# Performance work log

Measured on AMD Instinct MI355X. Metric: run time of the kernel, lower is better.

## Reference

```python
import jax, jax.numpy as jnp
import numpy as np

N, D = 16384, 256

def setup_inputs() -> dict:
    key = jax.random.key(0)
    k1, k2 = jax.random.split(key)
    image_emb = jax.random.normal(k1, (N, D), dtype=jnp.float32)
    text_emb = jax.random.normal(k2, (N, D), dtype=jnp.float32)
    return {"image_emb": image_emb, "text_emb": text_emb}

def reference(image_emb, text_emb):
    n = image_emb.shape[0]
    # [n, n] similarity logits
    logits = image_emb @ text_emb.T
    labels = jnp.arange(n)
    # cross-entropy with diagonal labels: -log_softmax(logits)[i, i]
    logp_t = jax.nn.log_softmax(logits, axis=-1)        # image -> text (rows)
    logp_i = jax.nn.log_softmax(logits.T, axis=-1)      # text -> image (cols)
    loss_t = -logp_t[labels, labels]
    loss_i = -logp_i[labels, labels]
    loss = ((loss_i + loss_t) * 0.5).mean()
    return loss
```

## Files before the change

### kernel.cpp

```cpp
#include <hip/hip_runtime.h>
#include <hip/hip_bf16.h>

#define NN 16384
#define DD 256

typedef unsigned short u16;
typedef unsigned int u32;
typedef unsigned char u8;
typedef long i64;
typedef __attribute__((ext_vector_type(4))) float f32x4;
typedef __attribute__((ext_vector_type(4))) int i32x4;
typedef __attribute__((ext_vector_type(8))) int i32x8;

__global__ __launch_bounds__(256) void prep_kernel(
        const float* __restrict__ img, const float* __restrict__ txt,
        u8* __restrict__ A8, u8* __restrict__ B8,
        float* __restrict__ zbuf ,
        float* __restrict__ out) {
    __shared__ u32 sA[16 * 65 + 8];
    __shared__ u32 sB[16 * 65 + 8];
    const int t = threadIdx.x, bi = blockIdx.x;
    const float4* ib = (const float4*)img + ((size_t)bi << 10);
    const float4* tb = (const float4*)txt + ((size_t)bi << 10);
    const float S = 1.44269504088896f;
    #pragma unroll
    for (int k = 0; k < 4; ++k) {
        const int idx = (k << 8) + t;
        const int row = idx >> 6, col = idx & 63;
        float4 va = ib[idx];
        int pa = __builtin_amdgcn_cvt_pk_fp8_f32(va.x * S, va.y * S, 0, false);
        pa     = __builtin_amdgcn_cvt_pk_fp8_f32(va.z * S, va.w * S, pa, true);
        sA[row * 65 + col] = (u32)pa;
        float4 vb = tb[idx];
        int pb = __builtin_amdgcn_cvt_pk_fp8_f32(vb.x, vb.y, 0, false);
        pb     = __builtin_amdgcn_cvt_pk_fp8_f32(vb.z, vb.w, pb, true);
        sB[row * 65 + col] = (u32)pb;
    }
    __syncthreads();
    const int w = t >> 6, l = t & 63;
    const int k2 = w >> 1, jj = w & 1, qq = l >> 4, mm = l & 15;
    const int wb = mm * 65 + (k2 << 5) + (qq << 3) + (jj << 2);
    i32x4 oa = { (int)sA[wb], (int)sA[wb + 1], (int)sA[wb + 2], (int)sA[wb + 3] };
    i32x4 ob = { (int)sB[wb], (int)sB[wb + 1], (int)sB[wb + 2], (int)sB[wb + 3] };
    const size_t dst = ((size_t)(bi >> 3) << 15) + (k2 << 14) + ((size_t)(bi & 7) << 11)
                     + (jj << 10) + (qq << 8) + (mm << 4);
    *(i32x4*)(A8 + dst) = oa;
    *(i32x4*)(B8 + dst) = ob;
    const int gid = (bi << 8) + t;
    if (gid < 32768) zbuf[gid] = 0.0f;
    if (gid == 0) out[0] = 0.0f;
}

__global__ __launch_bounds__(256, 2) void gemm_lse_kernel(
        const u8* __restrict__ A8, const u8* __restrict__ B8,
        float* __restrict__ s_row, float* __restrict__ s_col,
        float* __restrict__ diag) {
    const int t = threadIdx.x;
    const int lane = t & 63;
    const int w = t >> 6;
    const int wr = w >> 1, wc = w & 1;
    const int q = lane >> 4, m = lane & 15;
    const int bi = blockIdx.x & 127;
    const int jg = blockIdx.x >> 7;
    const int row0 = bi << 7;

    const u8* Aw = A8 + ((size_t)bi << 15) + ((size_t)lane << 4);
    i32x8 areg[2][4];
    #pragma unroll
    for (int k2 = 0; k2 < 2; ++k2)
        #pragma unroll
        for (int rb = 0; rb < 4; ++rb) {
            const u8* p = Aw + (k2 << 14) + (((wr << 2) + rb) << 11);
            i32x4 lo = *(const i32x4*)(p);
            i32x4 hi = *(const i32x4*)(p + 1024);
            areg[k2][rb] = __builtin_shufflevector(lo, hi, 0, 1, 2, 3, 4, 5, 6, 7);
        }

    const f32x4 fzero = {0.f, 0.f, 0.f, 0.f};
    f32x4 accA[4][2], accB[4][2];
    f32x4 rp[4] = {fzero, fzero, fzero, fzero};
    float cpartT = 0.0f;

    const u8* Bw = B8 + (wc << 13) + ((size_t)lane << 4);

    i32x8 bfX[4], bfY[4];

    auto load_half = [&](i32x8 (&bf)[4], int jt_, int h) {
        const int ct = (jg << 4) | ((jt_ + bi) & 15);
        const u8* p = Bw + ((size_t)ct << 15) + (h << 12);
        #pragma unroll
        for (int k2 = 0; k2 < 2; ++k2) {
            const u8* pp = p + (k2 << 14);
            i32x4 lo0 = *(const i32x4*)(pp);
            i32x4 hi0 = *(const i32x4*)(pp + 1024);
            bf[k2 * 2 + 0] = __builtin_shufflevector(lo0, hi0, 0, 1, 2, 3, 4, 5, 6, 7);
            i32x4 lo1 = *(const i32x4*)(pp + 2048);
            i32x4 hi1 = *(const i32x4*)(pp + 3072);
            bf[k2 * 2 + 1] = __builtin_shufflevector(lo1, hi1, 0, 1, 2, 3, 4, 5, 6, 7);
        }
    };

    auto mfma_half = [&](f32x4 (&acc)[4][2], i32x8 (&bf)[4]) {
        const f32x4 cinit = {-144.f, -144.f, -144.f, -144.f};
        #pragma unroll
        for (int rb = 0; rb < 4; ++rb) {
            acc[rb][0] = __builtin_amdgcn_mfma_scale_f32_16x16x128_f8f6f4(
                areg[0][rb], bf[0], cinit, 0, 0, 0, 127, 0, 127);
            acc[rb][1] = __builtin_amdgcn_mfma_scale_f32_16x16x128_f8f6f4(
                areg[0][rb], bf[1], cinit, 0, 0, 0, 127, 0, 127);
        }
        #pragma unroll
        for (int rb = 0; rb < 4; ++rb) {
            acc[rb][0] = __builtin_amdgcn_mfma_scale_f32_16x16x128_f8f6f4(
                areg[1][rb], bf[2], acc[rb][0], 0, 0, 0, 127, 0, 127);
            acc[rb][1] = __builtin_amdgcn_mfma_scale_f32_16x16x128_f8f6f4(
                areg[1][rb], bf[3], acc[rb][1], 0, 0, 0, 127, 0, 127);
        }
    };

    auto epilogue_half = [&](f32x4 (&acc)[4][2], int jt_, int h) {
        const int ct = (jg << 4) | ((jt_ + bi) & 15);
        if (bi == ct && wr == wc) {
            #pragma unroll
            for (int rb = 0; rb < 4; ++rb)
                if ((rb >> 1) == h) {
                    #pragma unroll
                    for (int r = 0; r < 4; ++r)
                        if (m == ((q << 2) | r))
                            diag[row0 + (wr << 6) + (rb << 4) + m] = acc[rb][rb & 1][r];
                }
        }
        #pragma unroll
        for (int rb = 0; rb < 4; ++rb)
            #pragma unroll
            for (int cb = 0; cb < 2; ++cb)
                #pragma unroll
                for (int r = 0; r < 4; ++r)
                    acc[rb][cb][r] = __builtin_amdgcn_exp2f(acc[rb][cb][r]);
        #pragma unroll
        for (int rb = 0; rb < 4; ++rb)
            rp[rb] += acc[rb][0] + acc[rb][1];
        #pragma unroll
        for (int cb = 0; cb < 2; ++cb) {
            f32x4 s = (acc[0][cb] + acc[1][cb]) + (acc[2][cb] + acc[3][cb]);
            float v = (s[0] + s[1]) + (s[2] + s[3]);
            v += __shfl_xor(v, 16, 64);
            v += __shfl_xor(v, 32, 64);
            if (q == ((h << 1) | cb)) cpartT = v;
        }
        if (h == 1) {
            const int col0 = ct << 7;
            atomicAdd(&s_col[col0 + (wc << 6) + (q << 4) + m], cpartT);
        }
    };

    load_half(bfX, 0, 0);
    load_half(bfY, 0, 1);
    mfma_half(accA, bfX);
    load_half(bfX, 1, 0);
    mfma_half(accB, bfY);
    epilogue_half(accA, 0, 0);
    #pragma unroll 1
    for (int jt = 1; jt < 16; ++jt) {
        load_half(bfY, jt, 1);
        mfma_half(accA, bfX);
        epilogue_half(accB, jt - 1, 1);
        if (jt < 15) load_half(bfX, jt + 1, 0);
        mfma_half(accB, bfY);
        epilogue_half(accA, jt, 0);
    }
    epilogue_half(accB, 15, 1);

    float rout = 0.0f;
    #pragma unroll
    for (int rb = 0; rb < 4; ++rb)
        #pragma unroll
        for (int r = 0; r < 4; ++r) {
            float v = rp[rb][r];
            v += __shfl_xor(v, 1, 16);
            v += __shfl_xor(v, 2, 16);
            v += __shfl_xor(v, 4, 16);
            v += __shfl_xor(v, 8, 16);
            if (m == ((rb << 2) | r)) rout = v;
        }
    atomicAdd(&s_row[row0 + (wr << 6) + ((m >> 2) << 4) + (q << 2) + (m & 3)], rout);
}

__global__ void final_kernel(const float* __restrict__ s_row, const float* __restrict__ s_col,
                             const float* __restrict__ diag, float* __restrict__ out) {
    __shared__ double red[256];
    int t = threadIdx.x;
    int i = blockIdx.x * 256 + t;
    double p = 0.5 * (double)(log2f(s_row[i]) + log2f(s_col[i])) - (double)diag[i];
    red[t] = p;
    __syncthreads();
    for (int s = 128; s > 0; s >>= 1) {
        if (t < s) red[t] += red[t + s];
        __syncthreads();
    }
    if (t == 0) atomicAdd(out, (float)(red[0] * 0.6931471805599453 / (double)NN));
}

extern "C" void kernel_launch(void* const* d_in, const int* in_sizes, int n_in,
                              void* d_out, int out_size, void* d_ws, size_t ws_size,
                              hipStream_t stream) {
    const float* img = (const float*)d_in[0];
    const float* txt = (const float*)d_in[1];
    char* ws = (char*)d_ws;
    u8*    A8    = (u8*)ws;
    u8*    B8    = (u8*)(ws + 4194304);
    float* s_row = (float*)(ws + 8388608);
    float* s_col = (float*)(ws + 8388608 + 65536);
    float* diag  = (float*)(ws + 8388608 + 131072);
    float* out   = (float*)d_out;

    prep_kernel<<<1024, 256, 0, stream>>>(img, txt, A8, B8, s_row, out);
    gemm_lse_kernel<<<1024, 256, 0, stream>>>(A8, B8, s_row, s_col, diag);
    final_kernel<<<64, 256, 0, stream>>>(s_row, s_col, diag, out);
}
```

Measured before the change: 155.8 us.

## Warp-specialize GEMM-LSE kernel into MFMA producer and exp consumer warps

Splits each 512-thread block into four MFMA producer waves and four epilogue consumer waves. Producers write accumulator tiles to two LDS buffers, and consumers apply exp2 and the row/column reductions, with __syncthreads handing tiles between them. The grid shrinks to 256 blocks, each walking 64 column tiles instead of 16, so column-sum atomics per block rise while grid count falls. The aim is to overlap transcendental and reduction work with matrix math. In exchange it adds two block-wide barriers per tile and 64KB of LDS per block, which may cap occupancy and serialize the two roles.

```diff
diff --git a/kernel.cpp b/kernel.cpp
--- a/kernel.cpp
+++ b/kernel.cpp
@@ -51,139 +51,167 @@
     if (gid == 0) out[0] = 0.0f;
 }
 
-__global__ __launch_bounds__(256, 2) void gemm_lse_kernel(
+__global__ __launch_bounds__(512, 2) void gemm_lse_kernel(
         const u8* __restrict__ A8, const u8* __restrict__ B8,
         float* __restrict__ s_row, float* __restrict__ s_col,
         float* __restrict__ diag) {
+    __shared__ float hbuf0[8192];
+    __shared__ float hbuf1[8192];
+
     const int t = threadIdx.x;
     const int lane = t & 63;
     const int w = t >> 6;
-    const int wr = w >> 1, wc = w & 1;
+    const int pw = w & 3;
+    const int wr = pw >> 1, wc = pw & 1;
     const int q = lane >> 4, m = lane & 15;
     const int bi = blockIdx.x & 127;
     const int jg = blockIdx.x >> 7;
     const int row0 = bi << 7;
 
-    const u8* Aw = A8 + ((size_t)bi << 15) + ((size_t)lane << 4);
-    i32x8 areg[2][4];
-    #pragma unroll
-    for (int k2 = 0; k2 < 2; ++k2)
+    if (w < 4) {
+        const u8* Aw = A8 + ((size_t)bi << 15) + ((size_t)lane << 4);
+        i32x8 areg[2][4];
         #pragma unroll
-        for (int rb = 0; rb < 4; ++rb) {
-            const u8* p = Aw + (k2 << 14) + (((wr << 2) + rb) << 11);
-            i32x4 lo = *(const i32x4*)(p);
-            i32x4 hi = *(const i32x4*)(p + 1024);
-            areg[k2][rb] = __builtin_shufflevector(lo, hi, 0, 1, 2, 3, 4, 5, 6, 7);
+        for (int k2 = 0; k2 < 2; ++k2)
+            #pragma unroll
+            for (int rb = 0; rb < 4; ++rb) {
+                const u8* p = Aw + (k2 << 14) + (((wr << 2) + rb) << 11);
+                i32x4 lo = *(const i32x4*)(p);
+                i32x4 hi = *(const i32x4*)(p + 1024);
+                areg[k2][rb] = __builtin_shufflevector(lo, hi, 0, 1, 2, 3, 4, 5, 6, 7);
+            }
+        const u8* Bw = B8 + (wc << 13) + ((size_t)lane << 4);
+        i32x8 bfX[4], bfY[4];
+        auto load_half = [&](i32x8 (&bf)[4], int jt_, int h) {
+            const int ct = (jg << 6) | ((jt_ + bi) & 63);
+            const u8* p = Bw + ((size_t)ct << 15) + (h << 12);
+            #pragma unroll
+            for (int k2 = 0; k2 < 2; ++k2) {
+                const u8* pp = p + (k2 << 14);
+                i32x4 lo0 = *(const i32x4*)(pp);
+                i32x4 hi0 = *(const i32x4*)(pp + 1024);
+                bf[k2 * 2 + 0] = __builtin_shufflevector(lo0, hi0, 0, 1, 2, 3, 4, 5, 6, 7);
+                i32x4 lo1 = *(const i32x4*)(pp + 2048);
+                i32x4 hi1 = *(const i32x4*)(pp + 3072);
+                bf[k2 * 2 + 1] = __builtin_shufflevector(lo1, hi1, 0, 1, 2, 3, 4, 5, 6, 7);
+            }
+        };
+        auto mfma_half = [&](f32x4 (&acc)[4][2], i32x8 (&bf)[4]) {
+            const f32x4 cinit = {-144.f, -144.f, -144.f, -144.f};
+            #pragma unroll
+            for (int rb = 0; rb < 4; ++rb) {
+                acc[rb][0] = __builtin_amdgcn_mfma_scale_f32_16x16x128_f8f6f4(
+                    areg[0][rb], bf[0], cinit, 0, 0, 0, 127, 0, 127);
+                acc[rb][1] = __builtin_amdgcn_mfma_scale_f32_16x16x128_f8f6f4(
+                    areg[0][rb], bf[1], cinit, 0, 0, 0, 127, 0, 127);
+            }
+            #pragma unroll
+            for (int rb = 0; rb < 4; ++rb) {
+                acc[rb][0] = __builtin_amdgcn_mfma_scale_f32_16x16x128_f8f6f4(
+                    areg[1][rb], bf[2], acc[rb][0], 0, 0, 0, 127, 0, 127);
+                acc[rb][1] = __builtin_amdgcn_mfma_scale_f32_16x16x128_f8f6f4(
+                    areg[1][rb], bf[3], acc[rb][1], 0, 0, 0, 127, 0, 127);
+            }
+        };
+        float* myb0 = hbuf0 + (pw << 11) + (lane << 2);
+        float* myb1 = hbuf1 + (pw << 11) + (lane << 2);
+        f32x4 acc[4][2];
+
+        load_half(bfX, 0, 0);
+        #pragma unroll 1
+        for (int jt = 0; jt < 64; ++jt) {
+            load_half(bfY, jt, 1);
+            mfma_half(acc, bfX);
+            #pragma unroll
+            for (int rb = 0; rb < 4; ++rb)
+                #pragma unroll
+                for (int cb = 0; cb < 2; ++cb)
+                    *(f32x4*)(myb0 + (((rb << 1) | cb) << 8)) = acc[rb][cb];
+            __syncthreads();
+            if (jt < 63) load_half(bfX, jt + 1, 0);
+            mfma_half(acc, bfY);
+            #pragma unroll
+            for (int rb = 0; rb < 4; ++rb)
+                #pragma unroll
+                for (int cb = 0; cb < 2; ++cb)
+                    *(f32x4*)(myb1 + (((rb << 1) | cb) << 8)) = acc[rb][cb];
+            __syncthreads();
         }
-
-    const f32x4 fzero = {0.f, 0.f, 0.f, 0.f};
-    f32x4 accA[4][2], accB[4][2];
-    f32x4 rp[4] = {fzero, fzero, fzero, fzero};
-    float cpartT = 0.0f;
-
-    const u8* Bw = B8 + (wc << 13) + ((size_t)lane << 4);
-
-    i32x8 bfX[4], bfY[4];
-
-    auto load_half = [&](i32x8 (&bf)[4], int jt_, int h) {
-        const int ct = (jg << 4) | ((jt_ + bi) & 15);
-        const u8* p = Bw + ((size_t)ct << 15) + (h << 12);
-        #pragma unroll
-        for (int k2 = 0; k2 < 2; ++k2) {
-            const u8* pp = p + (k2 << 14);
-            i32x4 lo0 = *(const i32x4*)(pp);
-            i32x4 hi0 = *(const i32x4*)(pp + 1024);
-            bf[k2 * 2 + 0] = __builtin_shufflevector(lo0, hi0, 0, 1, 2, 3, 4, 5, 6, 7);
-            i32x4 lo1 = *(const i32x4*)(pp + 2048);
-            i32x4 hi1 = *(const i32x4*)(pp + 3072);
-            bf[k2 * 2 + 1] = __builtin_shufflevector(lo1, hi1, 0, 1, 2, 3, 4, 5, 6, 7);
-        }
-    };
-
-    auto mfma_half = [&](f32x4 (&acc)[4][2], i32x8 (&bf)[4]) {
-        const f32x4 cinit = {-144.f, -144.f, -144.f, -144.f};
-        #pragma unroll
-        for (int rb = 0; rb < 4; ++rb) {
-            acc[rb][0] = __builtin_amdgcn_mfma_scale_f32_16x16x128_f8f6f4(
-                areg[0][rb], bf[0], cinit, 0, 0, 0, 127, 0, 127);
-            acc[rb][1] = __builtin_amdgcn_mfma_scale_f32_16x16x128_f8f6f4(
-                areg[0][rb], bf[1], cinit, 0, 0, 0, 127, 0, 127);
-        }
-        #pragma unroll
-        for (int rb = 0; rb < 4; ++rb) {
-            acc[rb][0] = __builtin_amdgcn_mfma_scale_f32_16x16x128_f8f6f4(
-                areg[1][rb], bf[2], acc[rb][0], 0, 0, 0, 127, 0, 127);
-            acc[rb][1] = __builtin_amdgcn_mfma_scale_f32_16x16x128_f8f6f4(
-                areg[1][rb], bf[3], acc[rb][1], 0, 0, 0, 127, 0, 127);
-        }
-    };
-
-    auto epilogue_half = [&](f32x4 (&acc)[4][2], int jt_, int h) {
-        const int ct = (jg << 4) | ((jt_ + bi) & 15);
-        if (bi == ct && wr == wc) {
-            #pragma unroll
-            for (int rb = 0; rb < 4; ++rb)
-                if ((rb >> 1) == h) {
+    } else {
+        const f32x4 fzero = {0.f, 0.f, 0.f, 0.f};
+        f32x4 rp[4] = {fzero, fzero, fzero, fzero};
+        float cpartT = 0.0f;
+        const float* myr0 = hbuf0 + (pw << 11) + (lane << 2);
+        const float* myr1 = hbuf1 + (pw << 11) + (lane << 2);
+
+        auto consume = [&](const float* src, int jt_, int h) {
+            const int ct = (jg << 6) | ((jt_ + bi) & 63);
+            f32x4 ev[4][2];
+            #pragma unroll
+            for (int rb = 0; rb < 4; ++rb)
+                #pragma unroll
+                for (int cb = 0; cb < 2; ++cb)
+                    ev[rb][cb] = *(const f32x4*)(src + (((rb << 1) | cb) << 8));
+            if (bi == ct && wr == wc) {
+                #pragma unroll
+                for (int rb = 0; rb < 4; ++rb)
+                    if ((rb >> 1) == h) {
+                        #pragma unroll
+                        for (int r = 0; r < 4; ++r)
+                            if (m == ((q << 2) | r))
+                                diag[row0 + (wr << 6) + (rb << 4) + m] = ev[rb][rb & 1][r];
+                    }
+            }
+            #pragma unroll
+            for (int rb = 0; rb < 4; ++rb)
+                #pragma unroll
+                for (int cb = 0; cb < 2; ++cb)
                     #pragma unroll
                     for (int r = 0; r < 4; ++r)
-                        if (m == ((q << 2) | r))
-                            diag[row0 + (wr << 6) + (rb << 4) + m] = acc[rb][rb & 1][r];
-                }
+                        ev[rb][cb][r] = __builtin_amdgcn_exp2f(ev[rb][cb][r]);
+            #pragma unroll
+            for (int rb = 0; rb < 4; ++rb)
+                rp[rb] += ev[rb][0] + ev[rb][1];
+            #pragma unroll
+            for (int cb = 0; cb < 2; ++cb) {
+                f32x4 s = (ev[0][cb] + ev[1][cb]) + (ev[2][cb] + ev[3][cb]);
+                float v = (s[0] + s[1]) + (s[2] + s[3]);
+                v += __shfl_xor(v, 16, 64);
+                v += __shfl_xor(v, 32, 64);
+                if (q == ((h << 1) | cb)) cpartT = v;
+            }
+            if (h == 1) {
+                const int col0 = ct << 7;
+                atomicAdd(&s_col[col0 + (wc << 6) + (q << 4) + m], cpartT);
+            }
+        };
+
+        __syncthreads();
+        #pragma unroll 1
+        for (int jt = 0; jt < 64; ++jt) {
+            consume(myr0, jt, 0);
+            __syncthreads();
+            if (jt < 63) {
+                consume(myr1, jt, 1);
+                __syncthreads();
+            }
         }
+        consume(myr1, 63, 1);
+
+        float rout = 0.0f;
         #pragma unroll
         for (int rb = 0; rb < 4; ++rb)
             #pragma unroll
-            for (int cb = 0; cb < 2; ++cb)
-                #pragma unroll
-                for (int r = 0; r < 4; ++r)
-                    acc[rb][cb][r] = __builtin_amdgcn_exp2f(acc[rb][cb][r]);
-        #pragma unroll
-        for (int rb = 0; rb < 4; ++rb)
-            rp[rb] += acc[rb][0] + acc[rb][1];
-        #pragma unroll
-        for (int cb = 0; cb < 2; ++cb) {
-            f32x4 s = (acc[0][cb] + acc[1][cb]) + (acc[2][cb] + acc[3][cb]);
-            float v = (s[0] + s[1]) + (s[2] + s[3]);
-            v += __shfl_xor(v, 16, 64);
-            v += __shfl_xor(v, 32, 64);
-            if (q == ((h << 1) | cb)) cpartT = v;
-        }
-        if (h == 1) {
-            const int col0 = ct << 7;
-            atomicAdd(&s_col[col0 + (wc << 6) + (q << 4) + m], cpartT);
-        }
-    };
-
-    load_half(bfX, 0, 0);
-    load_half(bfY, 0, 1);
-    mfma_half(accA, bfX);
-    load_half(bfX, 1, 0);
-    mfma_half(accB, bfY);
-    epilogue_half(accA, 0, 0);
-    #pragma unroll 1
-    for (int jt = 1; jt < 16; ++jt) {
-        load_half(bfY, jt, 1);
-        mfma_half(accA, bfX);
-        epilogue_half(accB, jt - 1, 1);
-        if (jt < 15) load_half(bfX, jt + 1, 0);
-        mfma_half(accB, bfY);
-        epilogue_half(accA, jt, 0);
+            for (int r = 0; r < 4; ++r) {
+                float v = rp[rb][r];
+                v += __shfl_xor(v, 1, 16);
+                v += __shfl_xor(v, 2, 16);
+                v += __shfl_xor(v, 4, 16);
+                v += __shfl_xor(v, 8, 16);
+                if (m == ((rb << 2) | r)) rout = v;
+            }
+        atomicAdd(&s_row[row0 + (wr << 6) + ((m >> 2) << 4) + (q << 2) + (m & 3)], rout);
     }
-    epilogue_half(accB, 15, 1);
-
-    float rout = 0.0f;
-    #pragma unroll
-    for (int rb = 0; rb < 4; ++rb)
-        #pragma unroll
-        for (int r = 0; r < 4; ++r) {
-            float v = rp[rb][r];
-            v += __shfl_xor(v, 1, 16);
-            v += __shfl_xor(v, 2, 16);
-            v += __shfl_xor(v, 4, 16);
-            v += __shfl_xor(v, 8, 16);
-            if (m == ((rb << 2) | r)) rout = v;
-        }
-    atomicAdd(&s_row[row0 + (wr << 6) + ((m >> 2) << 4) + (q << 2) + (m & 3)], rout);
 }
 
 __global__ void final_kernel(const float* __restrict__ s_row, const float* __restrict__ s_col,
@@ -215,6 +243,6 @@
     float* out   = (float*)d_out;
 
     prep_kernel<<<1024, 256, 0, stream>>>(img, txt, A8, B8, s_row, out);
-    gemm_lse_kernel<<<1024, 256, 0, stream>>>(A8, B8, s_row, s_col, diag);
+    gemm_lse_kernel<<<256, 512, 0, stream>>>(A8, B8, s_row, s_col, diag);
     final_kernel<<<64, 256, 0, stream>>>(s_row, s_col, diag, out);
 }
```

Result: slower. 165.3 us (+6.1%).
